# Performance work log

Hardware: AMD Instinct MI355X
Metric: run time of the kernel (lower is better)

## Reference

```python
import jax, jax.numpy as jnp
import numpy as np

B, S, D, K = 4, 2048, 1024, 8

def setup_inputs() -> dict:
    key = jax.random.key(0)
    k1, k2, k3 = jax.random.split(key, 3)
    hidden_states = jax.random.normal(k1, (B, S, D), dtype=jnp.float32)
    # scaled so scores ~ O(1) and exp() does not overflow
    W_phi = jax.random.normal(k2, (D, D), dtype=jnp.float32) * 0.005
    W_psi = jax.random.normal(k3, (D, D), dtype=jnp.float32) * 0.005
    return {"hidden_states": hidden_states, "W_phi": W_phi, "W_psi": W_psi, "k": K}

def reference(hidden_states, W_phi, W_psi, k):
    b, s, d = hidden_states.shape
    k = min(k, s)
    # nn.Linear(bias=False): y = x @ W.T
    phi_h = hidden_states @ W_phi.T            # [b,s,d]
    psi_h = hidden_states @ W_psi.T            # [b,s,d]
    scores = jnp.einsum('bsd,btd->bst', phi_h, psi_h)  # [b,s,s]
    affinity = jnp.exp(scores)
    topk_values, topk_indices = jax.lax.top_k(affinity, k)   # [b,s,k]
    norm_sum = topk_values.sum(axis=-1, keepdims=True) + 1e-8
    normalized_weights = topk_values / norm_sum
    batch_offset = (jnp.arange(b) * s)[:, None, None]        # [b,1,1]
    src_local = jnp.arange(s)[None, :, None]                 # [1,s,1]
    src_global = jnp.broadcast_to(batch_offset + src_local, (b, s, k))
    dst_global = batch_offset + topk_indices
    mask = (topk_indices != src_local).reshape(-1)           # drop self-loops
    # eager boolean compaction (data-dependent size, like the torch module)
    src_final = src_global.reshape(-1)[mask]
    dst_final = dst_global.reshape(-1)[mask]
    weights_final = normalized_weights.reshape(-1)[mask]
    if src_final.size == 0:
        all_nodes = jnp.arange(b * s)
        return jnp.stack([all_nodes, all_nodes], axis=0), jnp.ones(b * s, dtype=jnp.float32)
    edge_index = jnp.stack([src_final, dst_final], axis=0)
    return edge_index, weights_final
```

## Files before the change

### kernel.cpp

```cpp
#include <hip/hip_runtime.h>
#include <cmath>

#define SEQ 2048
#define DDIM 1024
#define NROWS 8192
#define KSEL 8
#define IMAXC 0x7fffffff

typedef __attribute__((ext_vector_type(8))) short bf16x8;
typedef __attribute__((ext_vector_type(4))) float f32x4;
typedef __attribute__((ext_vector_type(4))) double f64x4;

__device__ __forceinline__ unsigned short f2bf(float f) {
  unsigned u = __builtin_bit_cast(unsigned, f);
  u = (u + 0x7fffu + ((u >> 16) & 1u)) >> 16;
  return (unsigned short)u;
}
__device__ __forceinline__ float bf2f(unsigned short h) {
  unsigned u = ((unsigned)h) << 16;
  return __builtin_bit_cast(float, u);
}
__device__ __forceinline__ unsigned pkbf(float a, float b) {
  unsigned r;
  asm("v_cvt_pk_bf16_f32 %0, %1, %2" : "=v"(r) : "v"(a), "v"(b));
  return r;
}
__device__ __forceinline__ void dmap(int sel, int lg, int lr, int rg,
                                     int& ri, int& ci) {
  switch (sel) {
    case 0:  ri = (lg << 2) + rg; ci = lr; break;
    case 1:  ri = lg + (rg << 2); ci = lr; break;
    case 2:  ri = lr; ci = (lg << 2) + rg; break;
    default: ri = lr; ci = lg + (rg << 2); break;
  }
}

__global__ void kprobe(int* __restrict__ sel) {
  const int lane = threadIdx.x;
  const int lr = lane & 15, lg = lane >> 4;
  const double a = (double)(4 * lr + lg + 1);
  const double b = (double)(9 * lr + 5 * lg + 2);
  f64x4 d = (f64x4){0.0, 0.0, 0.0, 0.0};
  d = __builtin_amdgcn_mfma_f64_16x16x4f64(a, b, d, 0, 0, 0);
  int my = 4;
  for (int s = 3; s >= 0; --s) {
    bool ok = true;
    for (int rg = 0; rg < 4; ++rg) {
      int ri, ci;
      dmap(s, lg, lr, rg, ri, ci);
      double e = 0.0;
      for (int k = 0; k < 4; ++k)
        e += (double)(4 * ri + k + 1) * (double)(9 * ci + 5 * k + 2);
      ok = ok && (d[rg] == e);
    }
    if (__all(ok)) my = s;
  }
  if (lane == 0) sel[0] = my;
}

#define K0_STAGE(bi)                                        \
  do {                                                      \
    *reinterpret_cast<float4*>(&As[bi][kr][c4]) = pa0;      \
    *reinterpret_cast<float4*>(&As[bi][kr][c4 + 32]) = pa1; \
    *reinterpret_cast<float4*>(&Bs[bi][kr][c4]) = pb0;      \
    *reinterpret_cast<float4*>(&Bs[bi][kr][c4 + 32]) = pb1; \
  } while (0)

__global__ __launch_bounds__(256, 2)
void k0_mfma(const float* __restrict__ A, const float* __restrict__ B,
             float* __restrict__ C, const int* __restrict__ selp) {
  const int sel = selp[0];
  if (sel >= 4) return;
  __shared__ float As[2][32][72];
  __shared__ float Bs[2][32][72];
  const int tid = threadIdx.x;
  const int lane = tid & 63, w = tid >> 6;
  const int wr = w >> 1, wc = w & 1;
  const int lr = lane & 15, lg = lane >> 4;
  const int brow = blockIdx.y << 6, bcol = blockIdx.x << 6;
  const int kr = tid >> 3, c4 = (tid & 7) << 2;

  f64x4 acc[2][2];
#pragma unroll
  for (int mi = 0; mi < 2; ++mi)
#pragma unroll
    for (int nj = 0; nj < 2; ++nj)
      acc[mi][nj] = (f64x4){0.0, 0.0, 0.0, 0.0};

  const float* Ap = &A[(size_t)kr * DDIM + brow + c4];
  const float* Bp = &B[(size_t)kr * DDIM + bcol + c4];
  float4 pa0 = *reinterpret_cast<const float4*>(Ap);
  float4 pa1 = *reinterpret_cast<const float4*>(Ap + 32);
  float4 pb0 = *reinterpret_cast<const float4*>(Bp);
  float4 pb1 = *reinterpret_cast<const float4*>(Bp + 32);
  K0_STAGE(0);
  {
    const size_t nk = (size_t)32 * DDIM;
    pa0 = *reinterpret_cast<const float4*>(Ap + nk);
    pa1 = *reinterpret_cast<const float4*>(Ap + nk + 32);
    pb0 = *reinterpret_cast<const float4*>(Bp + nk);
    pb1 = *reinterpret_cast<const float4*>(Bp + nk + 32);
  }

  for (int t = 0; t < 32; ++t) {
    __syncthreads();
    const int cur = t & 1;
    if (t < 31) {
      K0_STAGE(cur ^ 1);
      if (t < 30) {
        const size_t nk = (size_t)(t + 2) * 32 * DDIM;
        pa0 = *reinterpret_cast<const float4*>(Ap + nk);
        pa1 = *reinterpret_cast<const float4*>(Ap + nk + 32);
        pb0 = *reinterpret_cast<const float4*>(Bp + nk);
        pb1 = *reinterpret_cast<const float4*>(Bp + nk + 32);
      }
    }
    __builtin_amdgcn_s_setprio(1);
#pragma unroll
    for (int kp = 0; kp < 8; ++kp) {
      const int ka = (kp << 2) + lg;
      double a[2], b[2];
#pragma unroll
      for (int mi = 0; mi < 2; ++mi)
        a[mi] = (double)As[cur][ka][(wr << 5) + (mi << 4) + lr];
#pragma unroll
      for (int nj = 0; nj < 2; ++nj)
        b[nj] = (double)Bs[cur][ka][(wc << 5) + (nj << 4) + lr];
#pragma unroll
      for (int mi = 0; mi < 2; ++mi)
#pragma unroll
        for (int nj = 0; nj < 2; ++nj)
          acc[mi][nj] = __builtin_amdgcn_mfma_f64_16x16x4f64(
              a[mi], b[nj], acc[mi][nj], 0, 0, 0);
    }
    __builtin_amdgcn_s_setprio(0);
  }
#pragma unroll
  for (int mi = 0; mi < 2; ++mi)
#pragma unroll
    for (int nj = 0; nj < 2; ++nj)
#pragma unroll
      for (int rg = 0; rg < 4; ++rg) {
        int ri, ci;
        dmap(sel, lg, lr, rg, ri, ci);
        C[(size_t)(brow + (wr << 5) + (mi << 4) + ri) * DDIM +
          bcol + (wc << 5) + (nj << 4) + ci] = (float)acc[mi][nj][rg];
      }
}

__global__ __launch_bounds__(256)
void k0_repair(const float* __restrict__ A, const float* __restrict__ B,
               float* __restrict__ C, const int* __restrict__ selp) {
  if (selp[0] < 4) return;
  __shared__ __align__(16) float As[32][68];
  __shared__ __align__(16) float Bs[32][68];
  const int tid = threadIdx.x;
  const int tx = tid & 15, ty = tid >> 4;
  const int brow = blockIdx.y << 6;
  const int bcol = blockIdx.x << 6;
  double acc[4][4] = {};
  for (int k0 = 0; k0 < DDIM; k0 += 32) {
#pragma unroll
    for (int i = 0; i < 2; ++i) {
      const int f = tid + (i << 8);
      const int r = f >> 4;
      const int c4 = (f & 15) << 2;
      *reinterpret_cast<float4*>(&As[r][c4]) =
          *reinterpret_cast<const float4*>(&A[(size_t)(k0 + r) * DDIM + brow + c4]);
      *reinterpret_cast<float4*>(&Bs[r][c4]) =
          *reinterpret_cast<const float4*>(&B[(size_t)(k0 + r) * DDIM + bcol + c4]);
    }
    __syncthreads();
#pragma unroll
    for (int kk = 0; kk < 32; ++kk) {
      const float4 a = *reinterpret_cast<const float4*>(&As[kk][ty << 2]);
      const float4 b = *reinterpret_cast<const float4*>(&Bs[kk][tx << 2]);
      const double ad[4] = {a.x, a.y, a.z, a.w};
      const double bd[4] = {b.x, b.y, b.z, b.w};
#pragma unroll
      for (int i = 0; i < 4; ++i)
#pragma unroll
        for (int j = 0; j < 4; ++j)
          acc[i][j] = fma(ad[i], bd[j], acc[i][j]);
    }
    __syncthreads();
  }
#pragma unroll
  for (int i = 0; i < 4; ++i) {
    float4 v = make_float4((float)acc[i][0], (float)acc[i][1],
                           (float)acc[i][2], (float)acc[i][3]);
    *reinterpret_cast<float4*>(
        &C[(size_t)(brow + (ty << 2) + i) * DDIM + bcol + (tx << 2)]) = v;
  }
}

#define K1_STAGE(bi)                                              \
  do {                                                            \
    As[bi][akh + 0][ar] = pa0.x; As[bi][akh + 1][ar] = pa0.y;     \
    As[bi][akh + 2][ar] = pa0.z; As[bi][akh + 3][ar] = pa0.w;     \
    As[bi][akh + 4][ar] = pa1.x; As[bi][akh + 5][ar] = pa1.y;     \
    As[bi][akh + 6][ar] = pa1.z; As[bi][akh + 7][ar] = pa1.w;     \
    *reinterpret_cast<float4*>(&Bs[bi][bk][bc4]) = pb0;           \
    *reinterpret_cast<float4*>(&Bs[bi][bk][bc4 + 64]) = pb1;      \
  } while (0)

__global__ __launch_bounds__(256, 2)
void k1_mfma(const float* __restrict__ A, const float* __restrict__ B,
             float* __restrict__ C, const int* __restrict__ selp) {
  const int sel = selp[0];
  if (sel >= 4) return;
  __shared__ float As[2][16][144];
  __shared__ float Bs[2][16][144];
  const int tid = threadIdx.x;
  const int lin = blockIdx.y * 8 + blockIdx.x;
  const int nlin = (lin & 7) * 64 + (lin >> 3);
  const int brow = (nlin >> 3) << 7;
  const int bcol = (nlin & 7) << 7;
  const int lane = tid & 63, w = tid >> 6;
  const int wr = w >> 1, wc = w & 1;
  const int lr = lane & 15, lg = lane >> 4;
  const int ar = tid >> 1, akh = (tid & 1) << 3;
  const int bk = tid >> 4, bc4 = (tid & 15) << 2;

  f64x4 acc[4][4];
#pragma unroll
  for (int mi = 0; mi < 4; ++mi)
#pragma unroll
    for (int nj = 0; nj < 4; ++nj)
      acc[mi][nj] = (f64x4){0.0, 0.0, 0.0, 0.0};

  const float* Ap = &A[(size_t)(brow + ar) * DDIM + akh];
  const float* Bp = &B[(size_t)bk * DDIM + bcol + bc4];

  float4 pa0 = *reinterpret_cast<const float4*>(Ap);
  float4 pa1 = *reinterpret_cast<const float4*>(Ap + 4);
  float4 pb0 = *reinterpret_cast<const float4*>(Bp);
  float4 pb1 = *reinterpret_cast<const float4*>(Bp + 64);
  K1_STAGE(0);
  pa0 = *reinterpret_cast<const float4*>(Ap + 16);
  pa1 = *reinterpret_cast<const float4*>(Ap + 20);
  pb0 = *reinterpret_cast<const float4*>(Bp + (size_t)16 * DDIM);
  pb1 = *reinterpret_cast<const float4*>(Bp + (size_t)16 * DDIM + 64);

  for (int t = 0; t < 64; ++t) {
    __syncthreads();
    const int cur = t & 1;
    if (t < 63) {
      K1_STAGE(cur ^ 1);
      if (t < 62) {
        const size_t ko = (size_t)(t + 2) << 4;
        pa0 = *reinterpret_cast<const float4*>(Ap + ko);
        pa1 = *reinterpret_cast<const float4*>(Ap + ko + 4);
        pb0 = *reinterpret_cast<const float4*>(Bp + ko * DDIM);
        pb1 = *reinterpret_cast<const float4*>(Bp + ko * DDIM + 64);
      }
    }
    __builtin_amdgcn_s_setprio(1);
#pragma unroll
    for (int kp = 0; kp < 4; ++kp) {
      const int ka = (kp << 2) + lg;
      double a[4], b[4];
#pragma unroll
      for (int mi = 0; mi < 4; ++mi)
        a[mi] = (double)As[cur][ka][(wr << 6) + (mi << 4) + lr];
#pragma unroll
      for (int nj = 0; nj < 4; ++nj)
        b[nj] = (double)Bs[cur][ka][(wc << 6) + (nj << 4) + lr];
#pragma unroll
      for (int mi = 0; mi < 4; ++mi)
#pragma unroll
        for (int nj = 0; nj < 4; ++nj)
          acc[mi][nj] = __builtin_amdgcn_mfma_f64_16x16x4f64(
              a[mi], b[nj], acc[mi][nj], 0, 0, 0);
    }
    __builtin_amdgcn_s_setprio(0);
  }
#pragma unroll
  for (int mi = 0; mi < 4; ++mi)
#pragma unroll
    for (int nj = 0; nj < 4; ++nj)
#pragma unroll
      for (int rg = 0; rg < 4; ++rg) {
        int ri, ci;
        dmap(sel, lg, lr, rg, ri, ci);
        C[(size_t)(brow + (wr << 6) + (mi << 4) + ri) * DDIM +
          bcol + (wc << 6) + (nj << 4) + ci] = (float)acc[mi][nj][rg];
      }
}

__global__ __launch_bounds__(256, 2)
void k1_repair(const float* __restrict__ A, const float* __restrict__ B,
               float* __restrict__ C, const int* __restrict__ selp) {
  if (selp[0] < 4) return;
  __shared__ double As[128][17];
  __shared__ double Bs[16][130];
  const int tid = threadIdx.x;
  const int lin = blockIdx.y * 8 + blockIdx.x;
  const int nlin = (lin & 7) * 64 + (lin >> 3);
  const int brow = (nlin >> 3) << 7;
  const int bcol = (nlin & 7) << 7;
  const int tx = tid & 15, ty = tid >> 4;
  const int ar = tid >> 1, aks = (tid & 1) << 3;
  const int bk = tid >> 4, btx = tid & 15;

  double acc[8][8];
#pragma unroll
  for (int i = 0; i < 8; ++i)
#pragma unroll
    for (int j = 0; j < 8; ++j) acc[i][j] = 0.0;

  const float* Aptr = &A[(size_t)(brow + ar) * DDIM + aks];
  const float* Bptr = &B[(size_t)bk * DDIM + bcol + (btx << 1)];

  float4 pa0, pa1;
  float2 pb[4];
  pa0 = *reinterpret_cast<const float4*>(Aptr);
  pa1 = *reinterpret_cast<const float4*>(Aptr + 4);
#pragma unroll
  for (int w = 0; w < 4; ++w)
    pb[w] = *reinterpret_cast<const float2*>(Bptr + (w << 5));

  for (int k0 = 0; k0 < DDIM; k0 += 16) {
    __syncthreads();
    As[ar][aks + 0] = (double)pa0.x; As[ar][aks + 1] = (double)pa0.y;
    As[ar][aks + 2] = (double)pa0.z; As[ar][aks + 3] = (double)pa0.w;
    As[ar][aks + 4] = (double)pa1.x; As[ar][aks + 5] = (double)pa1.y;
    As[ar][aks + 6] = (double)pa1.z; As[ar][aks + 7] = (double)pa1.w;
#pragma unroll
    for (int w = 0; w < 4; ++w) {
      Bs[bk][(btx << 1) + (w << 5) + 0] = (double)pb[w].x;
      Bs[bk][(btx << 1) + (w << 5) + 1] = (double)pb[w].y;
    }
    __syncthreads();
    if (k0 + 16 < DDIM) {
      pa0 = *reinterpret_cast<const float4*>(Aptr + k0 + 16);
      pa1 = *reinterpret_cast<const float4*>(Aptr + k0 + 20);
#pragma unroll
      for (int w = 0; w < 4; ++w)
        pb[w] = *reinterpret_cast<const float2*>(
            Bptr + (size_t)(k0 + 16) * DDIM + (w << 5));
    }
#pragma unroll 8
    for (int kk = 0; kk < 16; ++kk) {
      double a[8];
      double2 b[4];
#pragma unroll
      for (int i = 0; i < 8; ++i) a[i] = As[(ty << 3) + i][kk];
#pragma unroll
      for (int jj = 0; jj < 4; ++jj)
        b[jj] = *reinterpret_cast<const double2*>(&Bs[kk][(tx << 1) + (jj << 5)]);
#pragma unroll
      for (int i = 0; i < 8; ++i) {
#pragma unroll
        for (int jj = 0; jj < 4; ++jj) {
          acc[i][(jj << 1) + 0] = fma(a[i], b[jj].x, acc[i][(jj << 1) + 0]);
          acc[i][(jj << 1) + 1] = fma(a[i], b[jj].y, acc[i][(jj << 1) + 1]);
        }
      }
    }
  }
#pragma unroll
  for (int i = 0; i < 8; ++i) {
    float* crow = &C[(size_t)(brow + (ty << 3) + i) * DDIM + bcol + (tx << 1)];
#pragma unroll
    for (int jj = 0; jj < 4; ++jj) {
      float2 v = make_float2((float)acc[i][(jj << 1)],
                             (float)acc[i][(jj << 1) + 1]);
      *reinterpret_cast<float2*>(crow + (jj << 5)) = v;
    }
  }
}

#define K2_LOAD(koff)                                                         \
  do {                                                                        \
    _Pragma("unroll")                                                         \
    for (int q = 0; q < 4; ++q) {                                             \
      const int c = (q << 9) + tid;                                           \
      const int row = c >> 3;                                                 \
      const int gs = (c & 7) ^ (row & 7);                                     \
      const float* sT = &T[(size_t)(row0g + row) * DDIM + (koff) + (gs << 3)];\
      rT[2 * q] = *reinterpret_cast<const float4*>(sT);                       \
      rT[2 * q + 1] = *reinterpret_cast<const float4*>(sT + 4);               \
      const float* sH = &H[(size_t)(col0g + row) * DDIM + (koff) + (gs << 3)];\
      rH[2 * q] = *reinterpret_cast<const float4*>(sH);                       \
      rH[2 * q + 1] = *reinterpret_cast<const float4*>(sH + 4);               \
    }                                                                         \
  } while (0)

#define K2_STAGE(bi)                                                          \
  do {                                                                        \
    _Pragma("unroll")                                                         \
    for (int q = 0; q < 4; ++q) {                                             \
      const int c = (q << 9) + tid;                                           \
      uint4 o;                                                                \
      o.x = pkbf(rT[2 * q].x, rT[2 * q].y);                                   \
      o.y = pkbf(rT[2 * q].z, rT[2 * q].w);                                   \
      o.z = pkbf(rT[2 * q + 1].x, rT[2 * q + 1].y);                           \
      o.w = pkbf(rT[2 * q + 1].z, rT[2 * q + 1].w);                           \
      *reinterpret_cast<uint4*>(&u.stage[bi][0][c << 3]) = o;                 \
      uint4 o2;                                                               \
      o2.x = pkbf(rH[2 * q].x, rH[2 * q].y);                                  \
      o2.y = pkbf(rH[2 * q].z, rH[2 * q].w);                                  \
      o2.z = pkbf(rH[2 * q + 1].x, rH[2 * q + 1].y);                          \
      o2.w = pkbf(rH[2 * q + 1].z, rH[2 * q + 1].w);                          \
      *reinterpret_cast<uint4*>(&u.stage[bi][1][c << 3]) = o2;                \
    }                                                                         \
  } while (0)

__global__ __launch_bounds__(512, 1)
void k2_mfma(const float* __restrict__ T, const float* __restrict__ H,
             unsigned short* __restrict__ cand_v,
             unsigned char* __restrict__ cand_i) {
  __shared__ union {
    unsigned short stage[2][2][256 * 64];
    float Sl[64][264];
    struct {
      float mv[512][8];
      unsigned char mi[512][8];
    } mg;
  } u;
  const int tid = threadIdx.x;
  const int lane = tid & 63;
  const int w = tid >> 6;
  const int wr = w >> 2, wc = w & 3;
  const int lr = lane & 15, lg = lane >> 4;
  const int z = blockIdx.z;
  const int bx = blockIdx.x;
  const int brow = blockIdx.y << 8, bcol = bx << 8;
  const int row0g = z * SEQ + brow;
  const int col0g = z * SEQ + bcol;

  f32x4 acc[8][4];
#pragma unroll
  for (int mi = 0; mi < 8; ++mi)
#pragma unroll
    for (int nj = 0; nj < 4; ++nj)
      acc[mi][nj] = (f32x4){0.f, 0.f, 0.f, 0.f};

  float4 rT[8], rH[8];
  K2_LOAD(0);
  K2_STAGE(0);
  K2_LOAD(64);

  for (int t = 0; t < 16; ++t) {
    __syncthreads();
    const int cur = t & 1;
    if (t < 15) {
      K2_STAGE(cur ^ 1);
      if (t < 14) K2_LOAD((t + 2) << 6);
    }
#pragma unroll
    for (int kh = 0; kh < 2; ++kh) {
      const int sl = (kh << 2) + lg;
      bf16x8 bfv[4];
#pragma unroll
      for (int nj = 0; nj < 4; ++nj) {
        const int rb = (wc << 6) + (nj << 4) + lr;
        bfv[nj] = *reinterpret_cast<const bf16x8*>(
            &u.stage[cur][1][(rb << 6) + ((sl ^ (rb & 7)) << 3)]);
      }
#pragma unroll
      for (int mi = 0; mi < 8; ++mi) {
        const int ra = (wr << 7) + (mi << 4) + lr;
        const bf16x8 af = *reinterpret_cast<const bf16x8*>(
            &u.stage[cur][0][(ra << 6) + ((sl ^ (ra & 7)) << 3)]);
#pragma unroll
        for (int nj = 0; nj < 4; ++nj)
          acc[mi][nj] = __builtin_amdgcn_mfma_f32_16x16x32_bf16(
              af, bfv[nj], acc[mi][nj], 0, 0, 0);
      }
    }
  }

  const int srow = tid >> 3;
  const int qd = tid & 7;
#pragma unroll
  for (int p = 0; p < 4; ++p) {
    __syncthreads();
    if (wr == (p >> 1)) {
      const int mib = (p & 1) << 2;
#pragma unroll
      for (int mi2 = 0; mi2 < 4; ++mi2)
#pragma unroll
        for (int nj = 0; nj < 4; ++nj)
#pragma unroll
          for (int rg = 0; rg < 4; ++rg)
            u.Sl[(mi2 << 4) + (lg << 2) + rg][(wc << 6) + (nj << 4) + lr] =
                acc[mib + mi2][nj][rg];
    }
    __syncthreads();
    float v[KSEL];
    int ci[KSEL];
#pragma unroll
    for (int s = 0; s < KSEL; ++s) { v[s] = -3.0e38f; ci[s] = 0; }
    const int c0 = qd << 5;
    for (int c = 0; c < 32; ++c) {
      const float x = u.Sl[srow][c0 + c];
      if (x > v[KSEL - 1]) {
        float pv = x; int pc = c0 + c;
#pragma unroll
        for (int s = 0; s < KSEL; ++s) {
          if (x > v[s]) {
            const float tv = v[s]; const int tc = ci[s];
            v[s] = pv; ci[s] = pc; pv = tv; pc = tc;
          }
        }
      }
    }
    __syncthreads();
#pragma unroll
    for (int s = 0; s < KSEL; ++s) {
      u.mg.mv[tid][s] = v[s];
      u.mg.mi[tid][s] = (unsigned char)ci[s];
    }
    __syncthreads();
    if (qd == 0) {
      float fv[KSEL];
      int fi[KSEL];
#pragma unroll
      for (int s = 0; s < KSEL; ++s) { fv[s] = -3.0e38f; fi[s] = 0; }
#pragma unroll
      for (int t2 = 0; t2 < 8; ++t2) {
#pragma unroll
        for (int s = 0; s < KSEL; ++s) {
          const float x = u.mg.mv[tid + t2][s];
          const int idx = u.mg.mi[tid + t2][s];
          if (x > fv[KSEL - 1]) {
            float pv = x; int pc = idx;
#pragma unroll
            for (int s2 = 0; s2 < KSEL; ++s2) {
              if (x > fv[s2]) {
                const float tv = fv[s2]; const int tc = fi[s2];
                fv[s2] = pv; fi[s2] = pc; pv = tv; pc = tc;
              }
            }
          }
        }
      }
      const size_t base =
          (size_t)(row0g + (p << 6) + srow) * 64 + ((size_t)bx << 3);
#pragma unroll
      for (int s = 0; s < KSEL; ++s) {
        cand_v[base + s] = f2bf(fv[s]);
        cand_i[base + s] = (unsigned char)fi[s];
      }
    }
  }
}

__global__ __launch_bounds__(256)
void kr_rescore(const float* __restrict__ T, const float* __restrict__ H,
                const unsigned short* __restrict__ cand_v,
                const unsigned char* __restrict__ cand_i,
                int* __restrict__ topi, float* __restrict__ topw,
                int* __restrict__ cnt) {
  const int tid = threadIdx.x, lane = tid & 63, w = tid >> 6;
  const int r = blockIdx.x * 4 + w;
  const int b = r >> 11, iloc = r & (SEQ - 1);

  const size_t cbase = (size_t)r * 64;
  float v0 = bf2f(cand_v[cbase + lane]);
  int i0 = ((lane >> 3) << 8) + cand_i[cbase + lane];
  int keep = 0;
  for (int rnd = 0; rnd < 16; ++rnd) {
    float m = v0;
#pragma unroll
    for (int off = 32; off >= 1; off >>= 1) m = fmaxf(m, __shfl_xor(m, off));
    const unsigned long long bm = __ballot(v0 == m);
    const int owner = __ffsll(bm) - 1;
    const int oi = __shfl(i0, owner);
    if (lane == owner) v0 = -3.0e38f;
    if (lane == rnd) keep = oi;
  }

  const float* Trow = T + (size_t)r * DDIM;
  float4 t4[4];
#pragma unroll
  for (int q = 0; q < 4; ++q)
    t4[q] = *reinterpret_cast<const float4*>(&Trow[(q << 8) + (lane << 2)]);

  float t8v[KSEL];
  int t8i[KSEL];
#pragma unroll
  for (int p = 0; p < KSEL; ++p) { t8v[p] = -1.0f; t8i[p] = IMAXC; }

  for (int c = 0; c < 16; ++c) {
    const int j = __shfl(keep, c);
    const float* Hrow = H + ((size_t)(b << 11) + j) * DDIM;
    double s = 0.0;
#pragma unroll
    for (int q = 0; q < 4; ++q) {
      const float4 h = *reinterpret_cast<const float4*>(&Hrow[(q << 8) + (lane << 2)]);
      s = fma((double)t4[q].x, (double)h.x, s);
      s = fma((double)t4[q].y, (double)h.y, s);
      s = fma((double)t4[q].z, (double)h.z, s);
      s = fma((double)t4[q].w, (double)h.w, s);
    }
#pragma unroll
    for (int off = 1; off < 64; off <<= 1) s += __shfl_xor(s, off);
    const float aff = expf((float)s);
    const bool g7 = (aff > t8v[KSEL - 1]) ||
                    (aff == t8v[KSEL - 1] && j < t8i[KSEL - 1]);
    if (g7) {
      float pv = aff; int pi = j;
#pragma unroll
      for (int p = 0; p < KSEL; ++p) {
        const bool g = (aff > t8v[p]) || (aff == t8v[p] && j < t8i[p]);
        if (g) {
          const float tv = t8v[p]; const int ti = t8i[p];
          t8v[p] = pv; t8i[p] = pi; pv = tv; pi = ti;
        }
      }
    }
  }
  if (lane == 0) {
    float sum = 0.0f;
#pragma unroll
    for (int p = 0; p < KSEL; ++p) sum += t8v[p];
    sum += 1e-8f;
    int c8 = KSEL;
#pragma unroll
    for (int p = 0; p < KSEL; ++p)
      if (t8i[p] == iloc) --c8;
    cnt[r] = c8;
#pragma unroll
    for (int p = 0; p < KSEL; ++p) {
      topi[(size_t)r * KSEL + p] = t8i[p];
      topw[(size_t)r * KSEL + p] = t8v[p] / sum;
    }
  }
}

__global__ __launch_bounds__(1024)
void k4_scan(const int* __restrict__ cnt, int* __restrict__ off) {
  __shared__ int part[1024];
  const int t = threadIdx.x;
  int loc[8];
  int s = 0;
#pragma unroll
  for (int i = 0; i < 8; ++i) { loc[i] = s; s += cnt[t * 8 + i]; }
  part[t] = s;
  __syncthreads();
  for (int d = 1; d < 1024; d <<= 1) {
    const int add = (t >= d) ? part[t - d] : 0;
    __syncthreads();
    part[t] += add;
    __syncthreads();
  }
  const int base = (t == 0) ? 0 : part[t - 1];
#pragma unroll
  for (int i = 0; i < 8; ++i) off[t * 8 + i] = base + loc[i];
}

__global__ __launch_bounds__(256)
void k5_emit(const int* __restrict__ topi, const float* __restrict__ topw,
             const int* __restrict__ off, float* __restrict__ out, int E) {
  const int r = blockIdx.x * 256 + threadIdx.x;
  if (r >= NROWS) return;
  const int o = off[r];
  const int sloc = r & (SEQ - 1);
  const int bbase = r & ~(SEQ - 1);
  int e = 0;
#pragma unroll
  for (int p = 0; p < KSEL; ++p) {
    const int id = topi[(size_t)r * KSEL + p];
    const float w = topw[(size_t)r * KSEL + p];
    if (id != sloc) {
      const int pos = o + e;
      if (pos < E) {
        out[pos] = (float)r;
        out[(size_t)E + pos] = (float)(bbase + id);
        out[2 * (size_t)E + pos] = w;
      }
      ++e;
    }
  }
}

extern "C" void kernel_launch(void* const* d_in, const int* in_sizes, int n_in,
                              void* d_out, int out_size, void* d_ws,
                              size_t ws_size, hipStream_t stream) {
  const float* H = (const float*)d_in[0];
  const float* Wphi = (const float*)d_in[1];
  const float* Wpsi = (const float*)d_in[2];
  float* out = (float*)d_out;
  const int E = out_size / 3;

  char* base = (char*)d_ws;
  float* T = (float*)base;
  char* regionX = base + 33554432;
  float* Wc = (float*)regionX;
  unsigned short* cand_v = (unsigned short*)regionX;
  unsigned char* cand_i = (unsigned char*)(regionX + 2097152);
  char* pp = regionX + 4194304;
  int* topi = (int*)pp;  pp += 262144;
  float* topw = (float*)pp; pp += 262144;
  int* cnt = (int*)pp;   pp += 32768;
  int* off = (int*)pp;   pp += 32768;
  int* sel = (int*)pp;

  kprobe<<<dim3(1), 64, 0, stream>>>(sel);
  k0_mfma<<<dim3(16, 16), 256, 0, stream>>>(Wphi, Wpsi, Wc, sel);
  k0_repair<<<dim3(16, 16), 256, 0, stream>>>(Wphi, Wpsi, Wc, sel);
  k1_mfma<<<dim3(8, 64), 256, 0, stream>>>(H, Wc, T, sel);
  k1_repair<<<dim3(8, 64), 256, 0, stream>>>(H, Wc, T, sel);
  k2_mfma<<<dim3(8, 8, 4), 512, 0, stream>>>(T, H, cand_v, cand_i);
  kr_rescore<<<dim3(NROWS / 4), 256, 0, stream>>>(T, H, cand_v, cand_i,
                                                  topi, topw, cnt);
  k4_scan<<<dim3(1), 1024, 0, stream>>>(cnt, off);
  k5_emit<<<dim3(NROWS / 256), 256, 0, stream>>>(topi, topw, off, out, E);
}
```

Measured before the change: 563.0 us.

## Merge k1 MFMA and repair kernels into hybrid split across blocks

Replaces the two mutually exclusive k1 kernels with one kernel that sends the first 256 tiles through the FP64 MFMA path and the remaining 256 tiles through the FP64 vector-FMA path, sharing LDS via a union. The intent is to use both the matrix cores and the vector ALUs at once for the H·Wc projection, and to drop one kernel launch. The risk is load imbalance between the two paths, plus higher register and LDS pressure from the union and both code paths, which could reduce occupancy.

```diff
diff --git a/kernel.cpp b/kernel.cpp
--- a/kernel.cpp
+++ b/kernel.cpp
@@ -194,179 +194,173 @@
   }
 }
 
-#define K1_STAGE(bi)                                              \
-  do {                                                            \
-    As[bi][akh + 0][ar] = pa0.x; As[bi][akh + 1][ar] = pa0.y;     \
-    As[bi][akh + 2][ar] = pa0.z; As[bi][akh + 3][ar] = pa0.w;     \
-    As[bi][akh + 4][ar] = pa1.x; As[bi][akh + 5][ar] = pa1.y;     \
-    As[bi][akh + 6][ar] = pa1.z; As[bi][akh + 7][ar] = pa1.w;     \
-    *reinterpret_cast<float4*>(&Bs[bi][bk][bc4]) = pb0;           \
-    *reinterpret_cast<float4*>(&Bs[bi][bk][bc4 + 64]) = pb1;      \
-  } while (0)
-
 __global__ __launch_bounds__(256, 2)
-void k1_mfma(const float* __restrict__ A, const float* __restrict__ B,
-             float* __restrict__ C, const int* __restrict__ selp) {
+void k1_hybrid(const float* __restrict__ A, const float* __restrict__ B,
+               float* __restrict__ C, const int* __restrict__ selp) {
+  __shared__ union {
+    struct { float As[2][16][144]; float Bs[2][16][144]; } m;
+    struct { double As[128][17]; double Bs[16][130]; } v;
+  } u;
   const int sel = selp[0];
-  if (sel >= 4) return;
-  __shared__ float As[2][16][144];
-  __shared__ float Bs[2][16][144];
   const int tid = threadIdx.x;
   const int lin = blockIdx.y * 8 + blockIdx.x;
   const int nlin = (lin & 7) * 64 + (lin >> 3);
   const int brow = (nlin >> 3) << 7;
   const int bcol = (nlin & 7) << 7;
-  const int lane = tid & 63, w = tid >> 6;
-  const int wr = w >> 1, wc = w & 1;
-  const int lr = lane & 15, lg = lane >> 4;
-  const int ar = tid >> 1, akh = (tid & 1) << 3;
-  const int bk = tid >> 4, bc4 = (tid & 15) << 2;
-
-  f64x4 acc[4][4];
-#pragma unroll
-  for (int mi = 0; mi < 4; ++mi)
-#pragma unroll
-    for (int nj = 0; nj < 4; ++nj)
-      acc[mi][nj] = (f64x4){0.0, 0.0, 0.0, 0.0};
-
-  const float* Ap = &A[(size_t)(brow + ar) * DDIM + akh];
-  const float* Bp = &B[(size_t)bk * DDIM + bcol + bc4];
-
-  float4 pa0 = *reinterpret_cast<const float4*>(Ap);
-  float4 pa1 = *reinterpret_cast<const float4*>(Ap + 4);
-  float4 pb0 = *reinterpret_cast<const float4*>(Bp);
-  float4 pb1 = *reinterpret_cast<const float4*>(Bp + 64);
-  K1_STAGE(0);
-  pa0 = *reinterpret_cast<const float4*>(Ap + 16);
-  pa1 = *reinterpret_cast<const float4*>(Ap + 20);
-  pb0 = *reinterpret_cast<const float4*>(Bp + (size_t)16 * DDIM);
-  pb1 = *reinterpret_cast<const float4*>(Bp + (size_t)16 * DDIM + 64);
-
-  for (int t = 0; t < 64; ++t) {
-    __syncthreads();
-    const int cur = t & 1;
-    if (t < 63) {
-      K1_STAGE(cur ^ 1);
-      if (t < 62) {
-        const size_t ko = (size_t)(t + 2) << 4;
-        pa0 = *reinterpret_cast<const float4*>(Ap + ko);
-        pa1 = *reinterpret_cast<const float4*>(Ap + ko + 4);
-        pb0 = *reinterpret_cast<const float4*>(Bp + ko * DDIM);
-        pb1 = *reinterpret_cast<const float4*>(Bp + ko * DDIM + 64);
-      }
-    }
-    __builtin_amdgcn_s_setprio(1);
-#pragma unroll
-    for (int kp = 0; kp < 4; ++kp) {
-      const int ka = (kp << 2) + lg;
-      double a[4], b[4];
-#pragma unroll
-      for (int mi = 0; mi < 4; ++mi)
-        a[mi] = (double)As[cur][ka][(wr << 6) + (mi << 4) + lr];
+  const bool mf = (sel < 4) && (lin < 256);
+
+  if (mf) {
+    const int lane = tid & 63, w = tid >> 6;
+    const int wr = w >> 1, wc = w & 1;
+    const int lr = lane & 15, lg = lane >> 4;
+    const int ar = tid >> 1, akh = (tid & 1) << 3;
+    const int bk = tid >> 4, bc4 = (tid & 15) << 2;
+
+    f64x4 acc[4][4];
+#pragma unroll
+    for (int mi = 0; mi < 4; ++mi)
 #pragma unroll
       for (int nj = 0; nj < 4; ++nj)
-        b[nj] = (double)Bs[cur][ka][(wc << 6) + (nj << 4) + lr];
-#pragma unroll
-      for (int mi = 0; mi < 4; ++mi)
+        acc[mi][nj] = (f64x4){0.0, 0.0, 0.0, 0.0};
+
+    const float* Ap = &A[(size_t)(brow + ar) * DDIM + akh];
+    const float* Bp = &B[(size_t)bk * DDIM + bcol + bc4];
+
+#define K1M_STAGE(bi)                                                      \
+    do {                                                                   \
+      u.m.As[bi][akh + 0][ar] = pa0.x; u.m.As[bi][akh + 1][ar] = pa0.y;    \
+      u.m.As[bi][akh + 2][ar] = pa0.z; u.m.As[bi][akh + 3][ar] = pa0.w;    \
+      u.m.As[bi][akh + 4][ar] = pa1.x; u.m.As[bi][akh + 5][ar] = pa1.y;    \
+      u.m.As[bi][akh + 6][ar] = pa1.z; u.m.As[bi][akh + 7][ar] = pa1.w;    \
+      *reinterpret_cast<float4*>(&u.m.Bs[bi][bk][bc4]) = pb0;              \
+      *reinterpret_cast<float4*>(&u.m.Bs[bi][bk][bc4 + 64]) = pb1;         \
+    } while (0)
+
+    float4 pa0 = *reinterpret_cast<const float4*>(Ap);
+    float4 pa1 = *reinterpret_cast<const float4*>(Ap + 4);
+    float4 pb0 = *reinterpret_cast<const float4*>(Bp);
+    float4 pb1 = *reinterpret_cast<const float4*>(Bp + 64);
+    K1M_STAGE(0);
+    pa0 = *reinterpret_cast<const float4*>(Ap + 16);
+    pa1 = *reinterpret_cast<const float4*>(Ap + 20);
+    pb0 = *reinterpret_cast<const float4*>(Bp + (size_t)16 * DDIM);
+    pb1 = *reinterpret_cast<const float4*>(Bp + (size_t)16 * DDIM + 64);
+
+    for (int t = 0; t < 64; ++t) {
+      __syncthreads();
+      const int cur = t & 1;
+      if (t < 63) {
+        K1M_STAGE(cur ^ 1);
+        if (t < 62) {
+          const size_t ko = (size_t)(t + 2) << 4;
+          pa0 = *reinterpret_cast<const float4*>(Ap + ko);
+          pa1 = *reinterpret_cast<const float4*>(Ap + ko + 4);
+          pb0 = *reinterpret_cast<const float4*>(Bp + ko * DDIM);
+          pb1 = *reinterpret_cast<const float4*>(Bp + ko * DDIM + 64);
+        }
+      }
+      __builtin_amdgcn_s_setprio(1);
+#pragma unroll
+      for (int kp = 0; kp < 4; ++kp) {
+        const int ka = (kp << 2) + lg;
+        double a[4], b[4];
+#pragma unroll
+        for (int mi = 0; mi < 4; ++mi)
+          a[mi] = (double)u.m.As[cur][ka][(wr << 6) + (mi << 4) + lr];
 #pragma unroll
         for (int nj = 0; nj < 4; ++nj)
-          acc[mi][nj] = __builtin_amdgcn_mfma_f64_16x16x4f64(
-              a[mi], b[nj], acc[mi][nj], 0, 0, 0);
-    }
-    __builtin_amdgcn_s_setprio(0);
-  }
-#pragma unroll
-  for (int mi = 0; mi < 4; ++mi)
-#pragma unroll
-    for (int nj = 0; nj < 4; ++nj)
-#pragma unroll
-      for (int rg = 0; rg < 4; ++rg) {
-        int ri, ci;
-        dmap(sel, lg, lr, rg, ri, ci);
-        C[(size_t)(brow + (wr << 6) + (mi << 4) + ri) * DDIM +
-          bcol + (wc << 6) + (nj << 4) + ci] = (float)acc[mi][nj][rg];
-      }
-}
-
-__global__ __launch_bounds__(256, 2)
-void k1_repair(const float* __restrict__ A, const float* __restrict__ B,
-               float* __restrict__ C, const int* __restrict__ selp) {
-  if (selp[0] < 4) return;
-  __shared__ double As[128][17];
-  __shared__ double Bs[16][130];
-  const int tid = threadIdx.x;
-  const int lin = blockIdx.y * 8 + blockIdx.x;
-  const int nlin = (lin & 7) * 64 + (lin >> 3);
-  const int brow = (nlin >> 3) << 7;
-  const int bcol = (nlin & 7) << 7;
-  const int tx = tid & 15, ty = tid >> 4;
-  const int ar = tid >> 1, aks = (tid & 1) << 3;
-  const int bk = tid >> 4, btx = tid & 15;
-
-  double acc[8][8];
-#pragma unroll
-  for (int i = 0; i < 8; ++i)
-#pragma unroll
-    for (int j = 0; j < 8; ++j) acc[i][j] = 0.0;
-
-  const float* Aptr = &A[(size_t)(brow + ar) * DDIM + aks];
-  const float* Bptr = &B[(size_t)bk * DDIM + bcol + (btx << 1)];
-
-  float4 pa0, pa1;
-  float2 pb[4];
-  pa0 = *reinterpret_cast<const float4*>(Aptr);
-  pa1 = *reinterpret_cast<const float4*>(Aptr + 4);
-#pragma unroll
-  for (int w = 0; w < 4; ++w)
-    pb[w] = *reinterpret_cast<const float2*>(Bptr + (w << 5));
-
-  for (int k0 = 0; k0 < DDIM; k0 += 16) {
-    __syncthreads();
-    As[ar][aks + 0] = (double)pa0.x; As[ar][aks + 1] = (double)pa0.y;
-    As[ar][aks + 2] = (double)pa0.z; As[ar][aks + 3] = (double)pa0.w;
-    As[ar][aks + 4] = (double)pa1.x; As[ar][aks + 5] = (double)pa1.y;
-    As[ar][aks + 6] = (double)pa1.z; As[ar][aks + 7] = (double)pa1.w;
-#pragma unroll
-    for (int w = 0; w < 4; ++w) {
-      Bs[bk][(btx << 1) + (w << 5) + 0] = (double)pb[w].x;
-      Bs[bk][(btx << 1) + (w << 5) + 1] = (double)pb[w].y;
-    }
-    __syncthreads();
-    if (k0 + 16 < DDIM) {
-      pa0 = *reinterpret_cast<const float4*>(Aptr + k0 + 16);
-      pa1 = *reinterpret_cast<const float4*>(Aptr + k0 + 20);
-#pragma unroll
-      for (int w = 0; w < 4; ++w)
-        pb[w] = *reinterpret_cast<const float2*>(
-            Bptr + (size_t)(k0 + 16) * DDIM + (w << 5));
-    }
+          b[nj] = (double)u.m.Bs[cur][ka][(wc << 6) + (nj << 4) + lr];
+#pragma unroll
+        for (int mi = 0; mi < 4; ++mi)
+#pragma unroll
+          for (int nj = 0; nj < 4; ++nj)
+            acc[mi][nj] = __builtin_amdgcn_mfma_f64_16x16x4f64(
+                a[mi], b[nj], acc[mi][nj], 0, 0, 0);
+      }
+      __builtin_amdgcn_s_setprio(0);
+    }
+#pragma unroll
+    for (int mi = 0; mi < 4; ++mi)
+#pragma unroll
+      for (int nj = 0; nj < 4; ++nj)
+#pragma unroll
+        for (int rg = 0; rg < 4; ++rg) {
+          int ri, ci;
+          dmap(sel, lg, lr, rg, ri, ci);
+          C[(size_t)(brow + (wr << 6) + (mi << 4) + ri) * DDIM +
+            bcol + (wc << 6) + (nj << 4) + ci] = (float)acc[mi][nj][rg];
+        }
+  } else {
+    const int tx = tid & 15, ty = tid >> 4;
+    const int ar = tid >> 1, aks = (tid & 1) << 3;
+    const int bk = tid >> 4, btx = tid & 15;
+
+    double acc[8][8];
+#pragma unroll
+    for (int i = 0; i < 8; ++i)
+#pragma unroll
+      for (int j = 0; j < 8; ++j) acc[i][j] = 0.0;
+
+    const float* Aptr = &A[(size_t)(brow + ar) * DDIM + aks];
+    const float* Bptr = &B[(size_t)bk * DDIM + bcol + (btx << 1)];
+
+    float4 pa0, pa1;
+    float2 pb[4];
+    pa0 = *reinterpret_cast<const float4*>(Aptr);
+    pa1 = *reinterpret_cast<const float4*>(Aptr + 4);
+#pragma unroll
+    for (int w2 = 0; w2 < 4; ++w2)
+      pb[w2] = *reinterpret_cast<const float2*>(Bptr + (w2 << 5));
+
+    for (int k0 = 0; k0 < DDIM; k0 += 16) {
+      __syncthreads();
+      u.v.As[ar][aks + 0] = (double)pa0.x; u.v.As[ar][aks + 1] = (double)pa0.y;
+      u.v.As[ar][aks + 2] = (double)pa0.z; u.v.As[ar][aks + 3] = (double)pa0.w;
+      u.v.As[ar][aks + 4] = (double)pa1.x; u.v.As[ar][aks + 5] = (double)pa1.y;
+      u.v.As[ar][aks + 6] = (double)pa1.z; u.v.As[ar][aks + 7] = (double)pa1.w;
+#pragma unroll
+      for (int w2 = 0; w2 < 4; ++w2) {
+        u.v.Bs[bk][(btx << 1) + (w2 << 5) + 0] = (double)pb[w2].x;
+        u.v.Bs[bk][(btx << 1) + (w2 << 5) + 1] = (double)pb[w2].y;
+      }
+      __syncthreads();
+      if (k0 + 16 < DDIM) {
+        pa0 = *reinterpret_cast<const float4*>(Aptr + k0 + 16);
+        pa1 = *reinterpret_cast<const float4*>(Aptr + k0 + 20);
+#pragma unroll
+        for (int w2 = 0; w2 < 4; ++w2)
+          pb[w2] = *reinterpret_cast<const float2*>(
+              Bptr + (size_t)(k0 + 16) * DDIM + (w2 << 5));
+      }
 #pragma unroll 8
-    for (int kk = 0; kk < 16; ++kk) {
-      double a[8];
-      double2 b[4];
-#pragma unroll
-      for (int i = 0; i < 8; ++i) a[i] = As[(ty << 3) + i][kk];
-#pragma unroll
-      for (int jj = 0; jj < 4; ++jj)
-        b[jj] = *reinterpret_cast<const double2*>(&Bs[kk][(tx << 1) + (jj << 5)]);
-#pragma unroll
-      for (int i = 0; i < 8; ++i) {
-#pragma unroll
-        for (int jj = 0; jj < 4; ++jj) {
-          acc[i][(jj << 1) + 0] = fma(a[i], b[jj].x, acc[i][(jj << 1) + 0]);
-          acc[i][(jj << 1) + 1] = fma(a[i], b[jj].y, acc[i][(jj << 1) + 1]);
+      for (int kk = 0; kk < 16; ++kk) {
+        double a[8];
+        double2 b[4];
+#pragma unroll
+        for (int i = 0; i < 8; ++i) a[i] = u.v.As[(ty << 3) + i][kk];
+#pragma unroll
+        for (int jj = 0; jj < 4; ++jj)
+          b[jj] = *reinterpret_cast<const double2*>(
+              &u.v.Bs[kk][(tx << 1) + (jj << 5)]);
+#pragma unroll
+        for (int i = 0; i < 8; ++i) {
+#pragma unroll
+          for (int jj = 0; jj < 4; ++jj) {
+            acc[i][(jj << 1) + 0] = fma(a[i], b[jj].x, acc[i][(jj << 1) + 0]);
+            acc[i][(jj << 1) + 1] = fma(a[i], b[jj].y, acc[i][(jj << 1) + 1]);
+          }
         }
       }
     }
-  }
-#pragma unroll
-  for (int i = 0; i < 8; ++i) {
-    float* crow = &C[(size_t)(brow + (ty << 3) + i) * DDIM + bcol + (tx << 1)];
-#pragma unroll
-    for (int jj = 0; jj < 4; ++jj) {
-      float2 v = make_float2((float)acc[i][(jj << 1)],
-                             (float)acc[i][(jj << 1) + 1]);
-      *reinterpret_cast<float2*>(crow + (jj << 5)) = v;
+#pragma unroll
+    for (int i = 0; i < 8; ++i) {
+      float* crow = &C[(size_t)(brow + (ty << 3) + i) * DDIM + bcol + (tx << 1)];
+#pragma unroll
+      for (int jj = 0; jj < 4; ++jj) {
+        float2 v = make_float2((float)acc[i][(jj << 1)],
+                               (float)acc[i][(jj << 1) + 1]);
+        *reinterpret_cast<float2*>(crow + (jj << 5)) = v;
+      }
     }
   }
 }
@@ -702,8 +696,7 @@
   kprobe<<<dim3(1), 64, 0, stream>>>(sel);
   k0_mfma<<<dim3(16, 16), 256, 0, stream>>>(Wphi, Wpsi, Wc, sel);
   k0_repair<<<dim3(16, 16), 256, 0, stream>>>(Wphi, Wpsi, Wc, sel);
-  k1_mfma<<<dim3(8, 64), 256, 0, stream>>>(H, Wc, T, sel);
-  k1_repair<<<dim3(8, 64), 256, 0, stream>>>(H, Wc, T, sel);
+  k1_hybrid<<<dim3(8, 64), 256, 0, stream>>>(H, Wc, T, sel);
   k2_mfma<<<dim3(8, 8, 4), 512, 0, stream>>>(T, H, cand_v, cand_i);
   kr_rescore<<<dim3(NROWS / 4), 256, 0, stream>>>(T, H, cand_v, cand_i,
                                                   topi, topw, cnt);
```

Result: slower. 665.1 us (+18.1%).
